# Kernel tuning notes

Hardware: AMD Instinct MI355X
Metric: run time of the kernel (lower is better)

Reference implementation:

```python
import jax, jax.numpy as jnp
import numpy as np

ALPHA = 0.01  # matches LineFinderLoss(alpha=0.01)


def setup_inputs() -> dict:
    key = jax.random.key(0)
    k1, k2 = jax.random.split(key)
    S = 4096  # square so N == M == S (required for the original code to run)
    # column 4 is used as a probability: log(c) and log(1-c) must be finite
    inp = jax.random.uniform(k1, (S, S), dtype=jnp.float32, minval=1e-4, maxval=1.0 - 1e-4)
    tgt = jax.random.uniform(k2, (S, S), dtype=jnp.float32)
    return {"input": inp, "target": tgt}


def reference(input, target):
    N = input.shape[1]
    M = target.shape[1]
    # pairwise MSE cost over the first two coordinates: cost[n,m] = mean((input[n,:2]-target[m,:2])^2)
    diff = input[:, None, 0:2] - target[None, :, 0:2]  # [N, M, 2]
    cost = jnp.mean(diff * diff, axis=-1)              # [N, M]
    # Hungarian on an NxN cost yields a full assignment; the original code sets
    # X[p,l]=1 for the OUTER PRODUCT of matched row/col index sets, so X == ones
    # deterministically (matching does not affect the output).
    X = jnp.ones((N, M), dtype=input.dtype)
    mse_full = jnp.mean((input - target) ** 2)  # self.mse(input, target), constant over (n,m)
    log_c = jnpp_log = jnp.log(input[:, 4])     # [N]
    log_1mc = jnp.log(1.0 - input[:, 4])        # [N]
    # sum_{n,m} X*(alpha*mse_full - log c_n) - (1-X)*log(1-c_n)
    term = X * (ALPHA * mse_full - log_c[:, None]) - (1.0 - X) * log_1mc[:, None]
    # torch mse_loss(input[:,3], target) broadcasts (S,) against (S,S): elem [i,j] = (input[j,3]-target[i,j])^2
    loss = jnp.sum(term) + jnp.mean((input[:, 3] - target) ** 2)
    return loss, cost
```

## Files before the change

kernel.cpp:

```cpp
#include <hip/hip_runtime.h>

#define SDIM 4096
#define ALPHA 0.01f
#define WS_LOG 8
#define WS_ARR 128
#define WS_PART (WS_ARR + 5 * SDIM)


__global__ void k_gather(const float* __restrict__ inp, const float* __restrict__ tgt,
                         float* __restrict__ ws) {
    int n = blockIdx.x * 64 + threadIdx.x;
    const float* row = inp + (size_t)n * SDIM;
    const float* trow = tgt + (size_t)n * SDIM;
    float* arr = ws + WS_ARR;

    float v0 = row[0], v1 = row[1], v3 = row[3], v4 = row[4];
    arr[n]            = v0;
    arr[SDIM + n]     = v1;
    arr[2 * SDIM + n] = v3;
    arr[3 * SDIM + n] = trow[0];
    arr[4 * SDIM + n] = trow[1];

    float lg = logf(v4);
    #pragma unroll
    for (int off = 32; off > 0; off >>= 1) lg += __shfl_down(lg, off);
    if (threadIdx.x == 0) ws[WS_LOG + blockIdx.x] = lg;
}

__global__ void __launch_bounds__(256) k_main(const float* __restrict__ inp,
                                              const float* __restrict__ tgt,
                                              const float* __restrict__ ws,
                                              float* __restrict__ out,
                                              float* __restrict__ wpart) {
    __shared__ float s1[4], s2[4];
    const float* c0 = ws + WS_ARR;
    const float* c1 = c0 + SDIM;
    const float* c3 = c0 + 2 * SDIM;
    const float* t0 = c0 + 3 * SDIM;
    const float* t1 = c0 + 4 * SDIM;

    int n = blockIdx.x;
    int t = threadIdx.x;
    const float* irow = inp + (size_t)n * SDIM;
    const float* trow = tgt + (size_t)n * SDIM;
    float* orow = out + 1 + (size_t)n * SDIM;

    float4 vi[4], vt[4];
    #pragma unroll
    for (int k = 0; k < 4; ++k) {
        int col = (k * 256 + t) * 4;
        vi[k] = *(const float4*)(irow + col);
        vt[k] = *(const float4*)(trow + col);
    }
    float4 vc[4], w0[4], w1[4];
    #pragma unroll
    for (int k = 0; k < 4; ++k) {
        int col = (k * 256 + t) * 4;
        vc[k] = *(const float4*)(c3 + col);
        w0[k] = *(const float4*)(t0 + col);
        w1[k] = *(const float4*)(t1 + col);
    }
    float a0 = c0[n];
    float b0 = c1[n];

    float a1 = 0.0f, a2 = 0.0f;
    #pragma unroll
    for (int k = 0; k < 4; ++k) {
        int col = (k * 256 + t) * 4;
        float d, e0, e1;
        d = vi[k].x - vt[k].x; a1 += d * d;
        d = vi[k].y - vt[k].y; a1 += d * d;
        d = vi[k].z - vt[k].z; a1 += d * d;
        d = vi[k].w - vt[k].w; a1 += d * d;
        d = vc[k].x - vt[k].x; a2 += d * d;
        d = vc[k].y - vt[k].y; a2 += d * d;
        d = vc[k].z - vt[k].z; a2 += d * d;
        d = vc[k].w - vt[k].w; a2 += d * d;
        e0 = a0 - w0[k].x; e1 = b0 - w1[k].x; orow[col + 0] = 0.5f * (e0 * e0 + e1 * e1);
        e0 = a0 - w0[k].y; e1 = b0 - w1[k].y; orow[col + 1] = 0.5f * (e0 * e0 + e1 * e1);
        e0 = a0 - w0[k].z; e1 = b0 - w1[k].z; orow[col + 2] = 0.5f * (e0 * e0 + e1 * e1);
        e0 = a0 - w0[k].w; e1 = b0 - w1[k].w; orow[col + 3] = 0.5f * (e0 * e0 + e1 * e1);
    }

    #pragma unroll
    for (int off = 32; off > 0; off >>= 1) {
        a1 += __shfl_down(a1, off);
        a2 += __shfl_down(a2, off);
    }
    int wave = t >> 6;
    if ((t & 63) == 0) { s1[wave] = a1; s2[wave] = a2; }
    __syncthreads();
    if (t == 0) {
        wpart[n]        = s1[0] + s1[1] + s1[2] + s1[3];
        wpart[SDIM + n] = s2[0] + s2[1] + s2[2] + s2[3];
    }
}

__global__ void k_final(const float* __restrict__ ws, float* __restrict__ out) {
    __shared__ float s1[4], s2[4];
    float a1 = 0.0f, a2 = 0.0f;
    const float* wpart = ws + WS_PART;
    for (int i = threadIdx.x; i < SDIM; i += 256) {
        a1 += wpart[i];
        a2 += wpart[SDIM + i];
    }
    #pragma unroll
    for (int off = 32; off > 0; off >>= 1) {
        a1 += __shfl_down(a1, off);
        a2 += __shfl_down(a2, off);
    }
    int wave = threadIdx.x >> 6;
    if ((threadIdx.x & 63) == 0) { s1[wave] = a1; s2[wave] = a2; }
    __syncthreads();
    if (threadIdx.x == 0) {
        float sum_sq = s1[0] + s1[1] + s1[2] + s1[3];
        float sum3   = s2[0] + s2[1] + s2[2] + s2[3];
        float slog = 0.0f;
        #pragma unroll
        for (int i = 0; i < 64; ++i) slog += ws[WS_LOG + i];
        out[0] = ALPHA * sum_sq - (float)SDIM * slog
               + sum3 * (1.0f / ((float)SDIM * (float)SDIM));
    }
}

extern "C" void kernel_launch(void* const* d_in, const int* in_sizes, int n_in,
                              void* d_out, int out_size, void* d_ws, size_t ws_size,
                              hipStream_t stream) {
    const float* inp = (const float*)d_in[0];
    const float* tgt = (const float*)d_in[1];
    float* out = (float*)d_out;
    float* ws  = (float*)d_ws;

    k_gather<<<64, 64, 0, stream>>>(inp, tgt, ws);
    k_main<<<SDIM, 256, 0, stream>>>(inp, tgt, ws, out, ws + WS_PART);
    k_final<<<1, 256, 0, stream>>>(ws, out);
}
```

Before: 178.2 us.

## Tile main kernel as 8-row by 1024-column blocks to reuse column vectors

```diff
diff --git a/kernel.cpp b/kernel.cpp
--- a/kernel.cpp
+++ b/kernel.cpp
@@ -5,6 +5,7 @@
 #define WS_LOG 8
 #define WS_ARR 128
 #define WS_PART (WS_ARR + 5 * SDIM)
+#define NPART 2048
 
 
 __global__ void k_gather(const float* __restrict__ inp, const float* __restrict__ tgt,
@@ -39,47 +40,41 @@
     const float* t0 = c0 + 3 * SDIM;
     const float* t1 = c0 + 4 * SDIM;
 
-    int n = blockIdx.x;
     int t = threadIdx.x;
-    const float* irow = inp + (size_t)n * SDIM;
-    const float* trow = tgt + (size_t)n * SDIM;
-    float* orow = out + 1 + (size_t)n * SDIM;
+    int col = blockIdx.x * 1024 + t * 4;
+    int row0 = blockIdx.y * 8;
 
-    float4 vi[4], vt[4];
-    #pragma unroll
-    for (int k = 0; k < 4; ++k) {
-        int col = (k * 256 + t) * 4;
-        vi[k] = *(const float4*)(irow + col);
-        vt[k] = *(const float4*)(trow + col);
-    }
-    float4 vc[4], w0[4], w1[4];
-    #pragma unroll
-    for (int k = 0; k < 4; ++k) {
-        int col = (k * 256 + t) * 4;
-        vc[k] = *(const float4*)(c3 + col);
-        w0[k] = *(const float4*)(t0 + col);
-        w1[k] = *(const float4*)(t1 + col);
-    }
-    float a0 = c0[n];
-    float b0 = c1[n];
+    float4 f0 = *(const float4*)(t0 + col);
+    float4 f1 = *(const float4*)(t1 + col);
+    float4 fc = *(const float4*)(c3 + col);
 
     float a1 = 0.0f, a2 = 0.0f;
     #pragma unroll
-    for (int k = 0; k < 4; ++k) {
-        int col = (k * 256 + t) * 4;
-        float d, e0, e1;
-        d = vi[k].x - vt[k].x; a1 += d * d;
-        d = vi[k].y - vt[k].y; a1 += d * d;
-        d = vi[k].z - vt[k].z; a1 += d * d;
-        d = vi[k].w - vt[k].w; a1 += d * d;
-        d = vc[k].x - vt[k].x; a2 += d * d;
-        d = vc[k].y - vt[k].y; a2 += d * d;
-        d = vc[k].z - vt[k].z; a2 += d * d;
-        d = vc[k].w - vt[k].w; a2 += d * d;
-        e0 = a0 - w0[k].x; e1 = b0 - w1[k].x; orow[col + 0] = 0.5f * (e0 * e0 + e1 * e1);
-        e0 = a0 - w0[k].y; e1 = b0 - w1[k].y; orow[col + 1] = 0.5f * (e0 * e0 + e1 * e1);
-        e0 = a0 - w0[k].z; e1 = b0 - w1[k].z; orow[col + 2] = 0.5f * (e0 * e0 + e1 * e1);
-        e0 = a0 - w0[k].w; e1 = b0 - w1[k].w; orow[col + 3] = 0.5f * (e0 * e0 + e1 * e1);
+    for (int r = 0; r < 8; ++r) {
+        int n = row0 + r;
+        const float* irow = inp + (size_t)n * SDIM + col;
+        const float* trow = tgt + (size_t)n * SDIM + col;
+        float4 vi = *(const float4*)irow;
+        float4 vt = *(const float4*)trow;
+        float c0r = c0[n];
+        float c1r = c1[n];
+
+        float e0, e1;
+        float* orow = out + 1 + (size_t)n * SDIM + col;
+        e0 = c0r - f0.x; e1 = c1r - f1.x; orow[0] = 0.5f * (e0 * e0 + e1 * e1);
+        e0 = c0r - f0.y; e1 = c1r - f1.y; orow[1] = 0.5f * (e0 * e0 + e1 * e1);
+        e0 = c0r - f0.z; e1 = c1r - f1.z; orow[2] = 0.5f * (e0 * e0 + e1 * e1);
+        e0 = c0r - f0.w; e1 = c1r - f1.w; orow[3] = 0.5f * (e0 * e0 + e1 * e1);
+
+        float d;
+        d = vi.x - vt.x; a1 += d * d;
+        d = vi.y - vt.y; a1 += d * d;
+        d = vi.z - vt.z; a1 += d * d;
+        d = vi.w - vt.w; a1 += d * d;
+        d = fc.x - vt.x; a2 += d * d;
+        d = fc.y - vt.y; a2 += d * d;
+        d = fc.z - vt.z; a2 += d * d;
+        d = fc.w - vt.w; a2 += d * d;
     }
 
     #pragma unroll
@@ -91,8 +86,9 @@
     if ((t & 63) == 0) { s1[wave] = a1; s2[wave] = a2; }
     __syncthreads();
     if (t == 0) {
-        wpart[n]        = s1[0] + s1[1] + s1[2] + s1[3];
-        wpart[SDIM + n] = s2[0] + s2[1] + s2[2] + s2[3];
+        int idx = blockIdx.y * 4 + blockIdx.x;
+        wpart[idx]         = s1[0] + s1[1] + s1[2] + s1[3];
+        wpart[NPART + idx] = s2[0] + s2[1] + s2[2] + s2[3];
     }
 }
 
@@ -100,9 +96,9 @@
     __shared__ float s1[4], s2[4];
     float a1 = 0.0f, a2 = 0.0f;
     const float* wpart = ws + WS_PART;
-    for (int i = threadIdx.x; i < SDIM; i += 256) {
+    for (int i = threadIdx.x; i < NPART; i += 256) {
         a1 += wpart[i];
-        a2 += wpart[SDIM + i];
+        a2 += wpart[NPART + i];
     }
     #pragma unroll
     for (int off = 32; off > 0; off >>= 1) {
@@ -132,6 +128,6 @@
     float* ws  = (float*)d_ws;
 
     k_gather<<<64, 64, 0, stream>>>(inp, tgt, ws);
-    k_main<<<SDIM, 256, 0, stream>>>(inp, tgt, ws, out, ws + WS_PART);
+    k_main<<<dim3(4, 512), 256, 0, stream>>>(inp, tgt, ws, out, ws + WS_PART);
     k_final<<<1, 256, 0, stream>>>(ws, out);
 }
```

Result: slower. 182.3 us (+2.3%).
